# Kernel optimization log

Measured on AMD Instinct MI355X. Metric: run time of the kernel, lower is better.

The kernel has to match this reference:

```python
import jax, jax.numpy as jnp
import numpy as np

B, S, H = 4, 4096, 1024
NUM_LEVELS, DECAY = 3, 0.8
D0, D1 = 512, 204  # int(1024*0.5), int(512*0.5*0.8)


def _xavier(key, shape):
    fan_in, fan_out = shape
    return jax.random.normal(key, shape, dtype=jnp.float32) * np.sqrt(2.0 / (fan_in + fan_out))


def setup_inputs() -> dict:
    key = jax.random.key(0)
    ks = jax.random.split(key, 8)
    return {
        "keys": jax.random.normal(ks[0], (B, S, H), dtype=jnp.float32),
        "values": jax.random.normal(ks[1], (B, S, H), dtype=jnp.float32),
        "importance": jax.random.uniform(ks[2], (B, S), dtype=jnp.float32),
        # encoder layers (stored as [in, out]; torch Linear applies x @ W.T + b)
        "We0": _xavier(ks[3], (H, D0)), "be0": jnp.zeros((D0,), jnp.float32),
        "We1": _xavier(ks[4], (D0, D1)), "be1": jnp.zeros((D1,), jnp.float32),
        # decoder layers
        "Wd0": _xavier(ks[5], (D0, H)), "bd0": jnp.zeros((H,), jnp.float32),
        "Wd1": _xavier(ks[6], (D1, D0)), "bd1": jnp.zeros((D0,), jnp.float32),
    }


def _level_sizes(n):
    sizes, remaining = [], n
    for i in range(NUM_LEVELS):
        if i == NUM_LEVELS - 1:
            sizes.append(remaining)
        else:
            sz = int(remaining * (1 - DECAY) * DECAY ** i)
            sizes.append(sz)
            remaining -= sz
    return sizes


def reference(keys, values, importance, We0, be0, We1, be1, Wd0, bd0, Wd1, bd1):
    n = B * S
    fk = keys.reshape(n, H)
    fv = values.reshape(n, H)
    sorted_idx = jnp.argsort(-importance.reshape(-1))  # descending importance
    sizes = _level_sizes(n)

    def chain(x, level):
        # encode 0..level-1 with ReLU, then decode level-1..0 with ReLU
        if level >= 1:
            x = jax.nn.relu(x @ We0 + be0)
        if level >= 2:
            x = jax.nn.relu(x @ We1 + be1)
            x = jax.nn.relu(x @ Wd1 + bd1)
        if level >= 1:
            x = jax.nn.relu(x @ Wd0 + bd0)
        return x

    ck = jnp.zeros_like(fk)
    cv = jnp.zeros_like(fv)
    start = 0
    for level, size in enumerate(sizes):
        if size <= 0:
            continue
        idx = jax.lax.dynamic_slice(sorted_idx, (start,), (size,))
        ck = ck.at[idx].set(chain(fk[idx], level))
        cv = cv.at[idx].set(chain(fv[idx], level))
        start += size
    return ck.reshape(B, S, H), cv.reshape(B, S, H)
```

## Files before the change

kernel.cpp:

```cpp
#include <hip/hip_runtime.h>

typedef __attribute__((ext_vector_type(8))) short short8;
typedef __attribute__((ext_vector_type(4))) float f32x4;

#define N_TOK   16384
#define HDIM    1024
#define OUT_OFF 16777216
#define M1ROWS  26216
#define M2ROWS  22022
#define L2ROW0  4194

__device__ __forceinline__ unsigned short f2bf(float f) {
  unsigned int u = __float_as_uint(f);
  u += 0x7FFFu + ((u >> 16) & 1u);
  return (unsigned short)(u >> 16);
}

__device__ __forceinline__ void rowmap(int r, int& is_v, int& rank) {
  if (r < 2097)       { is_v = 0; rank = 3276 + r; }
  else if (r < 4194)  { is_v = 1; rank = 1179 + r; }
  else if (r < 15205) { is_v = 0; rank = 1179 + r; }
  else                { is_v = 1; rank = r - 9832; }
}

__global__ __launch_bounds__(256) void rank_count(const float* __restrict__ imp,
                                                  int* __restrict__ counts) {
  __shared__ float sj[2048];
  const int i = blockIdx.x * 256 + threadIdx.x;
  const int jbase = blockIdx.y * 2048;
  const float vi = imp[i];
  for (int s = threadIdx.x; s < 2048; s += 256) sj[s] = imp[jbase + s];
  __syncthreads();
  int cnt = 0;
  #pragma unroll 8
  for (int s = 0; s < 2048; ++s) {
    float vj = sj[s];
    bool gt = vj > vi;
    bool eq = (vj == vi) && ((jbase + s) < i);
    cnt += (gt || eq) ? 1 : 0;
  }
  atomicAdd(&counts[i], cnt);
}

__global__ __launch_bounds__(256) void scatter_order(const int* __restrict__ counts,
                                                     int* __restrict__ order) {
  int i = blockIdx.x * 256 + threadIdx.x;
  order[counts[i]] = i;
}

__global__ __launch_bounds__(256) void wconv(unsigned short* __restrict__ dst,
                                             const float* __restrict__ src,
                                             int Nd, int Kd, int Nsrc, int Ksrc) {
  int idx = blockIdx.x * 256 + threadIdx.x;
  if (idx >= Nd * Kd) return;
  int n = idx / Kd, k = idx % Kd;
  float v = (n < Nsrc && k < Ksrc) ? src[k * Nsrc + n] : 0.f;
  dst[idx] = f2bf(v);
}

__global__ __launch_bounds__(256) void gather_rows(unsigned short* __restrict__ X,
                                                   const float* __restrict__ keys,
                                                   const float* __restrict__ values,
                                                   const int* __restrict__ order) {
  int r = blockIdx.x;
  int is_v, rank; rowmap(r, is_v, rank);
  int token = order[rank];
  const float* src = (is_v ? values : keys) + (size_t)token * HDIM;
  int c = threadIdx.x * 4;
  float4 f = *reinterpret_cast<const float4*>(src + c);
  ushort4 h;
  h.x = f2bf(f.x); h.y = f2bf(f.y); h.z = f2bf(f.z); h.w = f2bf(f.w);
  *reinterpret_cast<ushort4*>(X + (size_t)r * HDIM + c) = h;
}

__global__ __launch_bounds__(256) void copy_level0(float* __restrict__ out,
                                                   const float* __restrict__ keys,
                                                   const float* __restrict__ values,
                                                   const int* __restrict__ order) {
  int b = blockIdx.x;
  int is_v = b & 1, rank = b >> 1;
  int token = order[rank];
  const float* src = (is_v ? values : keys) + (size_t)token * HDIM;
  float* dst = out + (is_v ? OUT_OFF : 0) + (size_t)token * HDIM;
  int c = threadIdx.x * 4;
  *reinterpret_cast<float4*>(dst + c) = *reinterpret_cast<const float4*>(src + c);
}

#define GLDS16(g, l) __builtin_amdgcn_global_load_lds( \
    (const __attribute__((address_space(1))) void*)(g), \
    (__attribute__((address_space(3))) void*)(l), 16, 0, 0)

template<int MODE>
__global__ __launch_bounds__(256) void gemm_bias_relu(
    const unsigned short* __restrict__ A, int M, int K,
    const unsigned short* __restrict__ Bt, int N,
    const float* __restrict__ bias, int Nbias,
    unsigned short* __restrict__ Cbf, int ldc,
    float* __restrict__ outf, const int* __restrict__ order) {
  __shared__ __align__(16) unsigned short As[128 * 32];
  __shared__ __align__(16) unsigned short Bs[128 * 32];
  const int tid = threadIdx.x;
  const int wave = tid >> 6, lane = tid & 63;
  const int row0 = blockIdx.x * 128, col0 = blockIdx.y * 128;
  const int lrow = lane >> 2, lk = (lane & 3) * 8;
  const int wr = (wave >> 1) * 64, wc = (wave & 1) * 64;

  const int s0 = wave * 2, s1 = wave * 2 + 1;
  int ar0 = row0 + s0 * 16 + lrow; if (ar0 >= M) ar0 = 0;
  int ar1 = row0 + s1 * 16 + lrow; if (ar1 >= M) ar1 = 0;
  int br0 = col0 + s0 * 16 + lrow; if (br0 >= N) br0 = 0;
  int br1 = col0 + s1 * 16 + lrow; if (br1 >= N) br1 = 0;
  const unsigned short* ap0 = A + (size_t)ar0 * K + lk;
  const unsigned short* ap1 = A + (size_t)ar1 * K + lk;
  const unsigned short* bp0 = Bt + (size_t)br0 * K + lk;
  const unsigned short* bp1 = Bt + (size_t)br1 * K + lk;

  f32x4 acc[4][4] = {};
  const int fr = lane & 15, fk = (lane >> 4) * 8;

  for (int k0 = 0; k0 < K; k0 += 32) {
    GLDS16(ap0 + k0, As + s0 * 512);
    GLDS16(ap1 + k0, As + s1 * 512);
    GLDS16(bp0 + k0, Bs + s0 * 512);
    GLDS16(bp1 + k0, Bs + s1 * 512);
    __syncthreads();
    short8 af[4], bfv[4];
    #pragma unroll
    for (int m = 0; m < 4; ++m)
      af[m] = *reinterpret_cast<const short8*>(As + (wr + m * 16 + fr) * 32 + fk);
    #pragma unroll
    for (int n = 0; n < 4; ++n)
      bfv[n] = *reinterpret_cast<const short8*>(Bs + (wc + n * 16 + fr) * 32 + fk);
    #pragma unroll
    for (int m = 0; m < 4; ++m)
      #pragma unroll
      for (int n = 0; n < 4; ++n)
        acc[m][n] = __builtin_amdgcn_mfma_f32_16x16x32_bf16(af[m], bfv[n], acc[m][n], 0, 0, 0);
    __syncthreads();
  }

  const int orow = (lane >> 4) * 4;
  const int ocol = lane & 15;
  #pragma unroll
  for (int m = 0; m < 4; ++m) {
    #pragma unroll
    for (int n = 0; n < 4; ++n) {
      #pragma unroll
      for (int j = 0; j < 4; ++j) {
        int r = row0 + wr + m * 16 + orow + j;
        int c = col0 + wc + n * 16 + ocol;
        if (r < M && c < N) {
          float v = acc[m][n][j] + (c < Nbias ? bias[c] : 0.f);
          v = fmaxf(v, 0.f);
          if (MODE == 0) {
            Cbf[(size_t)r * ldc + c] = f2bf(v);
          } else {
            int iv, rk; rowmap(r, iv, rk);
            int token = order[rk];
            outf[(size_t)(iv ? OUT_OFF : 0) + (size_t)token * HDIM + c] = v;
          }
        }
      }
    }
  }
}

extern "C" void kernel_launch(void* const* d_in, const int* in_sizes, int n_in,
                              void* d_out, int out_size, void* d_ws, size_t ws_size,
                              hipStream_t stream) {
  const float* keys   = (const float*)d_in[0];
  const float* values = (const float*)d_in[1];
  const float* imp    = (const float*)d_in[2];
  const float* We0    = (const float*)d_in[3];
  const float* be0    = (const float*)d_in[4];
  const float* We1    = (const float*)d_in[5];
  const float* be1    = (const float*)d_in[6];
  const float* Wd0    = (const float*)d_in[7];
  const float* bd0    = (const float*)d_in[8];
  const float* Wd1    = (const float*)d_in[9];
  const float* bd1    = (const float*)d_in[10];

  char* ws = (char*)d_ws;
  int* counts           = (int*)(ws);
  int* order            = (int*)(ws + 65536);
  unsigned short* We0T  = (unsigned short*)(ws + 131072);
  unsigned short* We1T  = (unsigned short*)(ws + 1179648);
  unsigned short* Wd1T  = (unsigned short*)(ws + 1409024);
  unsigned short* Wd0T  = (unsigned short*)(ws + 1638400);
  unsigned short* Y     = (unsigned short*)(ws + 2686976);
  unsigned short* Z     = (unsigned short*)(ws + 29532160);
  unsigned short* X = (unsigned short*)d_out;
  float* outf = (float*)d_out;

  hipMemsetAsync(counts, 0, 65536, stream);
  rank_count<<<dim3(64, 8), 256, 0, stream>>>(imp, counts);
  scatter_order<<<64, 256, 0, stream>>>(counts, order);

  wconv<<<2048, 256, 0, stream>>>(We0T, We0, 512, 1024, 512, 1024);
  wconv<<<448,  256, 0, stream>>>(We1T, We1, 224, 512, 204, 512);
  wconv<<<448,  256, 0, stream>>>(Wd1T, Wd1, 512, 224, 512, 204);
  wconv<<<2048, 256, 0, stream>>>(Wd0T, Wd0, 1024, 512, 1024, 512);

  gather_rows<<<M1ROWS, 256, 0, stream>>>(X, keys, values, order);

  gemm_bias_relu<0><<<dim3(205, 4), 256, 0, stream>>>(
      X, M1ROWS, 1024, We0T, 512, be0, 512, Y, 512, nullptr, nullptr);

  copy_level0<<<6552, 256, 0, stream>>>(outf, keys, values, order);

  gemm_bias_relu<0><<<dim3(173, 2), 256, 0, stream>>>(
      Y + (size_t)L2ROW0 * 512, M2ROWS, 512, We1T, 224, be1, 204, Z, 224, nullptr, nullptr);

  gemm_bias_relu<0><<<dim3(173, 4), 256, 0, stream>>>(
      Z, M2ROWS, 224, Wd1T, 512, bd1, 512, Y + (size_t)L2ROW0 * 512, 512, nullptr, nullptr);

  gemm_bias_relu<1><<<dim3(205, 8), 256, 0, stream>>>(
      Y, M1ROWS, 512, Wd0T, 1024, bd0, 1024, nullptr, 0, outf, order);
}
```

Baseline: 337.9 us.

## Double-buffer GEMM LDS tiles and XOR-swizzle k-chunks to avoid bank conflicts

The GEMM main loop now keeps two LDS buffers per operand and issues the global-to-LDS loads for the next k-tile before the MFMAs on the current tile run. This hides global load latency and leaves one barrier per iteration instead of two. The 16-byte k-chunk positions are also XOR-swizzled on both the store side and the read side to reduce LDS bank conflicts. In exchange the kernel uses twice the shared memory, which may lower occupancy. The swizzle only gives correct results if the write mapping and the read mapping agree exactly.

```diff
diff --git a/kernel.cpp b/kernel.cpp
--- a/kernel.cpp
+++ b/kernel.cpp
@@ -97,12 +97,13 @@
     const float* __restrict__ bias, int Nbias,
     unsigned short* __restrict__ Cbf, int ldc,
     float* __restrict__ outf, const int* __restrict__ order) {
-  __shared__ __align__(16) unsigned short As[128 * 32];
-  __shared__ __align__(16) unsigned short Bs[128 * 32];
+  __shared__ __align__(16) unsigned short As[2][128 * 32];
+  __shared__ __align__(16) unsigned short Bs[2][128 * 32];
   const int tid = threadIdx.x;
   const int wave = tid >> 6, lane = tid & 63;
   const int row0 = blockIdx.x * 128, col0 = blockIdx.y * 128;
-  const int lrow = lane >> 2, lk = (lane & 3) * 8;
+  const int lrow = lane >> 2;
+  const int lk = (((lane & 3) ^ ((lane >> 3) & 3)) << 3);
   const int wr = (wave >> 1) * 64, wc = (wave & 1) * 64;
 
   const int s0 = wave * 2, s1 = wave * 2 + 1;
@@ -116,27 +117,41 @@
   const unsigned short* bp1 = Bt + (size_t)br1 * K + lk;
 
   f32x4 acc[4][4] = {};
-  const int fr = lane & 15, fk = (lane >> 4) * 8;
-
-  for (int k0 = 0; k0 < K; k0 += 32) {
-    GLDS16(ap0 + k0, As + s0 * 512);
-    GLDS16(ap1 + k0, As + s1 * 512);
-    GLDS16(bp0 + k0, Bs + s0 * 512);
-    GLDS16(bp1 + k0, Bs + s1 * 512);
-    __syncthreads();
+  const int fr = lane & 15;
+  const int qoff = (((lane >> 4) ^ ((fr >> 1) & 3)) << 3);
+
+  const int nt = K >> 5;
+  GLDS16(ap0, As[0] + s0 * 512);
+  GLDS16(ap1, As[0] + s1 * 512);
+  GLDS16(bp0, Bs[0] + s0 * 512);
+  GLDS16(bp1, Bs[0] + s1 * 512);
+  __syncthreads();
+
+  int cur = 0;
+  for (int t = 0; t < nt; ++t) {
+    if (t + 1 < nt) {
+      const int k1 = (t + 1) << 5;
+      GLDS16(ap0 + k1, As[cur ^ 1] + s0 * 512);
+      GLDS16(ap1 + k1, As[cur ^ 1] + s1 * 512);
+      GLDS16(bp0 + k1, Bs[cur ^ 1] + s0 * 512);
+      GLDS16(bp1 + k1, Bs[cur ^ 1] + s1 * 512);
+    }
+    const unsigned short* as = As[cur];
+    const unsigned short* bs = Bs[cur];
     short8 af[4], bfv[4];
     #pragma unroll
     for (int m = 0; m < 4; ++m)
-      af[m] = *reinterpret_cast<const short8*>(As + (wr + m * 16 + fr) * 32 + fk);
+      af[m] = *reinterpret_cast<const short8*>(as + (wr + m * 16 + fr) * 32 + qoff);
     #pragma unroll
     for (int n = 0; n < 4; ++n)
-      bfv[n] = *reinterpret_cast<const short8*>(Bs + (wc + n * 16 + fr) * 32 + fk);
+      bfv[n] = *reinterpret_cast<const short8*>(bs + (wc + n * 16 + fr) * 32 + qoff);
     #pragma unroll
     for (int m = 0; m < 4; ++m)
       #pragma unroll
       for (int n = 0; n < 4; ++n)
         acc[m][n] = __builtin_amdgcn_mfma_f32_16x16x32_bf16(af[m], bfv[n], acc[m][n], 0, 0, 0);
     __syncthreads();
+    cur ^= 1;
   }
 
   const int orow = (lane >> 4) * 4;
```

Measured after the change: 330.9 us. 2.1% less time.

## Rewrite GEMMs as B-stationary LDS kernels with direct register A streaming

Applied to the files above, without the earlier changes.

Replaces the 128x128 LDS-tiled GEMM with a kernel that loads the whole weight column-panel (BN x K) into XOR-swizzled LDS once, then streams A rows from global directly into registers with double-buffered prefetch across 8 waves of 512-row tiles. Blocks are grouped in 8-row swizzles for L2 reuse, the hidden dimension is padded to 256, and X moves from the output buffer to workspace. The aim is to cut per-k-step barriers and repeated B loads. The trade-off is more LDS per block and A fragments read uncoalesced from global without LDS staging.

```diff
diff --git a/kernel.cpp b/kernel.cpp
--- a/kernel.cpp
+++ b/kernel.cpp
@@ -90,65 +90,105 @@
     (const __attribute__((address_space(1))) void*)(g), \
     (__attribute__((address_space(3))) void*)(l), 16, 0, 0)
 
-template<int MODE>
-__global__ __launch_bounds__(256) void gemm_bias_relu(
-    const unsigned short* __restrict__ A, int M, int K,
+template<int MODE, int MFR, int NFR, int K>
+__global__ __launch_bounds__(512) void bstat_gemm(
+    const unsigned short* __restrict__ A, int M,
     const unsigned short* __restrict__ Bt, int N,
     const float* __restrict__ bias, int Nbias,
     unsigned short* __restrict__ Cbf, int ldc,
-    float* __restrict__ outf, const int* __restrict__ order) {
-  __shared__ __align__(16) unsigned short As[128 * 32];
-  __shared__ __align__(16) unsigned short Bs[128 * 32];
+    float* __restrict__ outf, const int* __restrict__ order,
+    int NP, int NC) {
+  constexpr int BN = NFR * 16;
+  constexpr int CH = K / 8;
+  __shared__ __align__(16) unsigned short Blds[BN * K];
+
+  const int bid = blockIdx.x;
+  const int r8 = bid & 7, rest = bid >> 3;
+  const int c8 = rest % NC, q8 = rest / NC;
+  const int p8 = q8 * 8 + r8;
+  if (p8 >= NP) return;
+  const int row0 = p8 * 512;
+  const int col0 = c8 * BN;
+
   const int tid = threadIdx.x;
   const int wave = tid >> 6, lane = tid & 63;
-  const int row0 = blockIdx.x * 128, col0 = blockIdx.y * 128;
-  const int lrow = lane >> 2, lk = (lane & 3) * 8;
-  const int wr = (wave >> 1) * 64, wc = (wave & 1) * 64;
-
-  const int s0 = wave * 2, s1 = wave * 2 + 1;
-  int ar0 = row0 + s0 * 16 + lrow; if (ar0 >= M) ar0 = 0;
-  int ar1 = row0 + s1 * 16 + lrow; if (ar1 >= M) ar1 = 0;
-  int br0 = col0 + s0 * 16 + lrow; if (br0 >= N) br0 = 0;
-  int br1 = col0 + s1 * 16 + lrow; if (br1 >= N) br1 = 0;
-  const unsigned short* ap0 = A + (size_t)ar0 * K + lk;
-  const unsigned short* ap1 = A + (size_t)ar1 * K + lk;
-  const unsigned short* bp0 = Bt + (size_t)br0 * K + lk;
-  const unsigned short* bp1 = Bt + (size_t)br1 * K + lk;
-
-  f32x4 acc[4][4] = {};
-  const int fr = lane & 15, fk = (lane >> 4) * 8;
-
-  for (int k0 = 0; k0 < K; k0 += 32) {
-    GLDS16(ap0 + k0, As + s0 * 512);
-    GLDS16(ap1 + k0, As + s1 * 512);
-    GLDS16(bp0 + k0, Bs + s0 * 512);
-    GLDS16(bp1 + k0, Bs + s1 * 512);
-    __syncthreads();
-    short8 af[4], bfv[4];
-    #pragma unroll
-    for (int m = 0; m < 4; ++m)
-      af[m] = *reinterpret_cast<const short8*>(As + (wr + m * 16 + fr) * 32 + fk);
-    #pragma unroll
-    for (int n = 0; n < 4; ++n)
-      bfv[n] = *reinterpret_cast<const short8*>(Bs + (wc + n * 16 + fr) * 32 + fk);
-    #pragma unroll
-    for (int m = 0; m < 4; ++m)
-      #pragma unroll
-      for (int n = 0; n < 4; ++n)
-        acc[m][n] = __builtin_amdgcn_mfma_f32_16x16x32_bf16(af[m], bfv[n], acc[m][n], 0, 0, 0);
-    __syncthreads();
-  }
-
-  const int orow = (lane >> 4) * 4;
-  const int ocol = lane & 15;
-  #pragma unroll
-  for (int m = 0; m < 4; ++m) {
-    #pragma unroll
-    for (int n = 0; n < 4; ++n) {
+  const int fr = lane & 15, lch = lane >> 4;
+
+  constexpr int ROUNDS = (BN * K * 2) / 8192;
+  #pragma unroll
+  for (int j = 0; j < ROUNDS; ++j) {
+    int off16 = (j * 8 + wave) * 64 + lane;
+    int brow = off16 / CH;
+    int bslot = off16 % CH;
+    int bsrc = bslot ^ (brow & 7);
+    int gr = col0 + brow; if (gr >= N) gr = 0;
+    GLDS16(Bt + (size_t)gr * K + bsrc * 8, Blds + (size_t)off16 * 8);
+  }
+  asm volatile("s_waitcnt vmcnt(0)" ::: "memory");
+  __syncthreads();
+
+  const int arow = row0 + wave * 64;
+  const unsigned short* ap[MFR];
+  #pragma unroll
+  for (int m = 0; m < MFR; ++m) {
+    int rr = arow + m * 16 + fr; if (rr >= M) rr = 0;
+    ap[m] = A + (size_t)rr * K + lch * 8;
+  }
+
+  f32x4 acc[MFR][NFR] = {};
+  constexpr int NT = K / 32;
+  short8 a0[MFR], a1[MFR];
+  #pragma unroll
+  for (int m = 0; m < MFR; ++m) a0[m] = *reinterpret_cast<const short8*>(ap[m]);
+  #pragma unroll
+  for (int m = 0; m < MFR; ++m) a1[m] = *reinterpret_cast<const short8*>(ap[m] + 32);
+
+  #pragma unroll 1
+  for (int t = 0; t < NT; t += 2) {
+    short8 b[NFR];
+    #pragma unroll
+    for (int n = 0; n < NFR; ++n) {
+      int brow = n * 16 + fr;
+      int pc = (4 * t + lch) ^ (brow & 7);
+      b[n] = *reinterpret_cast<const short8*>(Blds + brow * K + pc * 8);
+    }
+    #pragma unroll
+    for (int m = 0; m < MFR; ++m)
+      #pragma unroll
+      for (int n = 0; n < NFR; ++n)
+        acc[m][n] = __builtin_amdgcn_mfma_f32_16x16x32_bf16(a0[m], b[n], acc[m][n], 0, 0, 0);
+    if (t + 2 < NT) {
+      #pragma unroll
+      for (int m = 0; m < MFR; ++m)
+        a0[m] = *reinterpret_cast<const short8*>(ap[m] + (t + 2) * 32);
+    }
+    #pragma unroll
+    for (int n = 0; n < NFR; ++n) {
+      int brow = n * 16 + fr;
+      int pc = (4 * (t + 1) + lch) ^ (brow & 7);
+      b[n] = *reinterpret_cast<const short8*>(Blds + brow * K + pc * 8);
+    }
+    #pragma unroll
+    for (int m = 0; m < MFR; ++m)
+      #pragma unroll
+      for (int n = 0; n < NFR; ++n)
+        acc[m][n] = __builtin_amdgcn_mfma_f32_16x16x32_bf16(a1[m], b[n], acc[m][n], 0, 0, 0);
+    if (t + 3 < NT) {
+      #pragma unroll
+      for (int m = 0; m < MFR; ++m)
+        a1[m] = *reinterpret_cast<const short8*>(ap[m] + (t + 3) * 32);
+    }
+  }
+
+  const int orow = lch * 4;
+  #pragma unroll
+  for (int m = 0; m < MFR; ++m) {
+    #pragma unroll
+    for (int n = 0; n < NFR; ++n) {
       #pragma unroll
       for (int j = 0; j < 4; ++j) {
-        int r = row0 + wr + m * 16 + orow + j;
-        int c = col0 + wc + n * 16 + ocol;
+        int r = arow + m * 16 + orow + j;
+        int c = col0 + n * 16 + fr;
         if (r < M && c < N) {
           float v = acc[m][n][j] + (c < Nbias ? bias[c] : 0.f);
           v = fmaxf(v, 0.f);
@@ -164,6 +204,8 @@
     }
   }
 }
+
+static inline int swzg(int NP, int NC) { return 8 * NC * ((NP + 7) / 8); }
 
 extern "C" void kernel_launch(void* const* d_in, const int* in_sizes, int n_in,
                               void* d_out, int out_size, void* d_ws, size_t ws_size,
@@ -185,11 +227,11 @@
   int* order            = (int*)(ws + 65536);
   unsigned short* We0T  = (unsigned short*)(ws + 131072);
   unsigned short* We1T  = (unsigned short*)(ws + 1179648);
-  unsigned short* Wd1T  = (unsigned short*)(ws + 1409024);
-  unsigned short* Wd0T  = (unsigned short*)(ws + 1638400);
-  unsigned short* Y     = (unsigned short*)(ws + 2686976);
-  unsigned short* Z     = (unsigned short*)(ws + 29532160);
-  unsigned short* X = (unsigned short*)d_out;
+  unsigned short* Wd1T  = (unsigned short*)(ws + 1441792);
+  unsigned short* Wd0T  = (unsigned short*)(ws + 1703936);
+  unsigned short* Y     = (unsigned short*)(ws + 2752512);
+  unsigned short* Z     = (unsigned short*)(ws + 29597696);
+  unsigned short* X     = (unsigned short*)(ws + 40872960);
   float* outf = (float*)d_out;
 
   hipMemsetAsync(counts, 0, 65536, stream);
@@ -197,23 +239,24 @@
   scatter_order<<<64, 256, 0, stream>>>(counts, order);
 
   wconv<<<2048, 256, 0, stream>>>(We0T, We0, 512, 1024, 512, 1024);
-  wconv<<<448,  256, 0, stream>>>(We1T, We1, 224, 512, 204, 512);
-  wconv<<<448,  256, 0, stream>>>(Wd1T, Wd1, 512, 224, 512, 204);
+  wconv<<<512,  256, 0, stream>>>(We1T, We1, 256, 512, 204, 512);
+  wconv<<<512,  256, 0, stream>>>(Wd1T, Wd1, 512, 256, 512, 204);
   wconv<<<2048, 256, 0, stream>>>(Wd0T, Wd0, 1024, 512, 1024, 512);
 
   gather_rows<<<M1ROWS, 256, 0, stream>>>(X, keys, values, order);
-
-  gemm_bias_relu<0><<<dim3(205, 4), 256, 0, stream>>>(
-      X, M1ROWS, 1024, We0T, 512, be0, 512, Y, 512, nullptr, nullptr);
-
   copy_level0<<<6552, 256, 0, stream>>>(outf, keys, values, order);
 
-  gemm_bias_relu<0><<<dim3(173, 2), 256, 0, stream>>>(
-      Y + (size_t)L2ROW0 * 512, M2ROWS, 512, We1T, 224, be1, 204, Z, 224, nullptr, nullptr);
-
-  gemm_bias_relu<0><<<dim3(173, 4), 256, 0, stream>>>(
-      Z, M2ROWS, 224, Wd1T, 512, bd1, 512, Y + (size_t)L2ROW0 * 512, 512, nullptr, nullptr);
-
-  gemm_bias_relu<1><<<dim3(205, 8), 256, 0, stream>>>(
-      Y, M1ROWS, 512, Wd0T, 1024, bd0, 1024, nullptr, 0, outf, order);
-}
+  bstat_gemm<0, 4, 4, 1024><<<swzg(52, 8), 512, 0, stream>>>(
+      X, M1ROWS, We0T, 512, be0, 512, Y, 512, nullptr, nullptr, 52, 8);
+
+  bstat_gemm<0, 4, 8, 512><<<swzg(44, 2), 512, 0, stream>>>(
+      Y + (size_t)L2ROW0 * 512, M2ROWS, We1T, 256, be1, 204, Z, 256,
+      nullptr, nullptr, 44, 2);
+
+  bstat_gemm<0, 4, 8, 256><<<swzg(44, 4), 512, 0, stream>>>(
+      Z, M2ROWS, Wd1T, 512, bd1, 512, Y + (size_t)L2ROW0 * 512, 512,
+      nullptr, nullptr, 44, 4);
+
+  bstat_gemm<1, 4, 8, 512><<<swzg(52, 8), 512, 0, stream>>>(
+      Y, M1ROWS, Wd0T, 1024, bd0, 1024, nullptr, 0, outf, order, 52, 8);
+}
```

After: 381.2 us. +12.8%, slower.
